# Performance work log

Measured on AMD Instinct MI355X. Metric: run time of the kernel, lower is better.

The kernel has to match this reference:

```python
import jax, jax.numpy as jnp
import numpy as np

D = 1024
HEADS = 16
HEAD_DIM = D // HEADS
B = 4
L = 1024


def setup_inputs() -> dict:
    key = jax.random.key(0)
    kq, kk, kv, kw, kb = jax.random.split(key, 5)
    Q = jax.random.normal(kq, (B, L, D), dtype=jnp.float32)
    K = jax.random.normal(kk, (B, L, D), dtype=jnp.float32)
    V = jax.random.normal(kv, (B, L, D), dtype=jnp.float32)
    # Output projection H: torch nn.Linear(D, D) -> weight (D, D), bias (D,)
    lim = 1.0 / np.sqrt(D)
    W_H = jax.random.uniform(kw, (D, D), minval=-lim, maxval=lim, dtype=jnp.float32)
    b_H = jax.random.uniform(kb, (D,), minval=-lim, maxval=lim, dtype=jnp.float32)
    mask = 0  # falsy -> no masking branch, matching `if mask` in the source
    return {"Q": Q, "K": K, "V": V, "W_H": W_H, "b_H": b_H, "mask": mask}


def reference(Q, K, V, W_H, b_H, mask):
    batch, q_len, _ = Q.shape
    k_len = K.shape[1]
    Qh = Q.reshape(batch, q_len, HEADS, HEAD_DIM)
    Kh = K.reshape(batch, k_len, HEADS, HEAD_DIM)
    Vh = V.reshape(batch, k_len, HEADS, HEAD_DIM)
    scores = jnp.einsum('bqhd,bkhd->bhqk', Qh, Kh)  # [B,H,Lq,Lk]
    if mask:  # mask is a Python scalar (0 -> skip), as in source
        scores = jnp.where(mask == 0, -jnp.inf, scores)
    # NOTE: source scales by sqrt(D), not sqrt(head_dim)
    attn = jax.nn.softmax(scores / np.sqrt(D).astype(np.float32), axis=3)
    out = jnp.einsum('bhql,blhd->bqhd', attn, Vh).reshape(batch, q_len, D)
    return out @ W_H.T + b_H
```

## Files before the change

kernel.cpp:

```cpp
#include <hip/hip_runtime.h>
#include <hip/hip_bf16.h>

typedef __attribute__((ext_vector_type(4))) float f32x4;
typedef __attribute__((ext_vector_type(8))) short bf16x8;

constexpr int Bn  = 4;
constexpr int Ln  = 1024;
constexpr int Dn  = 1024;
constexpr int Hn  = 16;
constexpr int HDn = 64;

static __device__ __forceinline__ unsigned short bf16r(float f) {
    union { float f; unsigned int u; } x;
    x.f = f;
    unsigned int r = x.u + 0x7fffu + ((x.u >> 16) & 1u);
    return (unsigned short)(r >> 16);
}

static __device__ __forceinline__ unsigned int pk2(float a, float b) {
    return (unsigned int)bf16r(a) | ((unsigned int)bf16r(b) << 16);
}

__global__ __launch_bounds__(256) void prep_kernel(
    const float* __restrict__ Vg, const float* __restrict__ Wg,
    unsigned short* __restrict__ Vtg, unsigned short* __restrict__ Wbf)
{
    const int tid = threadIdx.x;
    if (blockIdx.z == 4) {
        const int r0 = blockIdx.x * 64, c0 = blockIdx.y * 64;
#pragma unroll 4
        for (int i = 0; i < 4; ++i) {
            int e4 = i * 256 + tid;
            int r = e4 >> 4, c4 = e4 & 15;
            const float* p = Wg + (size_t)(r0 + r) * Dn + c0 + c4 * 4;
            float4 v = *(const float4*)p;
            ushort4 o;
            o.x = bf16r(v.x); o.y = bf16r(v.y); o.z = bf16r(v.z); o.w = bf16r(v.w);
            *(ushort4*)(Wbf + (size_t)(r0 + r) * Dn + c0 + c4 * 4) = o;
        }
        return;
    }

    __shared__ unsigned short T[64][72];
    const int k0 = blockIdx.x * 64;
    const int h  = blockIdx.y;
    const int b  = blockIdx.z;
    const float* Vb = Vg + (size_t)b * Ln * Dn + h * HDn;

#pragma unroll 4
    for (int i = 0; i < 4; ++i) {
        int e4 = i * 256 + tid;
        int r = e4 >> 4, c4 = e4 & 15;
        float4 vv = *(const float4*)(Vb + (size_t)(k0 + r) * Dn + c4 * 4);
        T[c4 * 4 + 0][r] = bf16r(vv.x);
        T[c4 * 4 + 1][r] = bf16r(vv.y);
        T[c4 * 4 + 2][r] = bf16r(vv.z);
        T[c4 * 4 + 3][r] = bf16r(vv.w);
    }
    __syncthreads();
    unsigned short* out = Vtg + ((size_t)(b * Hn + h) * HDn) * Ln + k0;
#pragma unroll 2
    for (int i = 0; i < 2; ++i) {
        int e8 = i * 256 + tid;
        int r = e8 >> 3, c8 = e8 & 7;
        *(uint4*)(out + (size_t)r * Ln + c8 * 8) = *(const uint4*)&T[r][c8 * 8];
    }
}

__global__ __launch_bounds__(512) void attn_kernel(
    const float* __restrict__ Qg, const float* __restrict__ Kg,
    const unsigned short* __restrict__ Vtg, unsigned short* __restrict__ Xg)
{
    __shared__ uint4 Ks4[2][64][8];
    __shared__ uint4 Vts4[2][64][8];
    __shared__ uint2 Ps2[256][16];

    const int tid  = threadIdx.x;
    const int wave = tid >> 6;
    const int lane = tid & 63;
    const int l16  = lane & 15;
    const int quad = lane >> 4;
    const int r7   = l16 & 7;
    const int wb   = wave * 32;

    const int flat = blockIdx.x;
    const int xcd  = flat & 7;
    const int j    = flat >> 3;
    const int qt   = j & 3;
    const int gg   = j >> 2;
    const int g    = xcd + 8 * gg;
    const int h    = g & 15;
    const int b    = g >> 4;
    const int q0   = qt * 256;

    const float* Kf   = Kg + (size_t)b * Ln * Dn + h * HDn;
    const uint4* Vtb4 = (const uint4*)(Vtg + ((size_t)(b * Hn + h) * HDn) * Ln);

    bf16x8 bq[2][2];
#pragma unroll 2
    for (int hf = 0; hf < 2; ++hf) {
        const float* qp = Qg + ((size_t)b * Ln + q0 + wb + hf * 16 + l16) * Dn
                             + h * HDn + quad * 8;
        float4 a0 = *(const float4*)qp;
        float4 a1 = *(const float4*)(qp + 4);
        float4 a2 = *(const float4*)(qp + 32);
        float4 a3 = *(const float4*)(qp + 36);
        bq[hf][0][0] = (short)bf16r(a0.x); bq[hf][0][1] = (short)bf16r(a0.y);
        bq[hf][0][2] = (short)bf16r(a0.z); bq[hf][0][3] = (short)bf16r(a0.w);
        bq[hf][0][4] = (short)bf16r(a1.x); bq[hf][0][5] = (short)bf16r(a1.y);
        bq[hf][0][6] = (short)bf16r(a1.z); bq[hf][0][7] = (short)bf16r(a1.w);
        bq[hf][1][0] = (short)bf16r(a2.x); bq[hf][1][1] = (short)bf16r(a2.y);
        bq[hf][1][2] = (short)bf16r(a2.z); bq[hf][1][3] = (short)bf16r(a2.w);
        bq[hf][1][4] = (short)bf16r(a3.x); bq[hf][1][5] = (short)bf16r(a3.y);
        bq[hf][1][6] = (short)bf16r(a3.z); bq[hf][1][7] = (short)bf16r(a3.w);
    }

    const float SC = 1.4426950408889634f / 32.0f;

    float lsum[2] = {0.f, 0.f};
    f32x4 Oacc[2][4];
#pragma unroll 2
    for (int hf = 0; hf < 2; ++hf)
#pragma unroll 4
        for (int d = 0; d < 4; ++d) Oacc[hf][d] = (f32x4){0.f, 0.f, 0.f, 0.f};

    const int sr = tid >> 3, sc = tid & 7;
    const int scs = sc ^ (sr & 7);
    float4 kr0, kr1;
    uint4 vreg;

    kr0 = *(const float4*)(Kf + (size_t)sr * Dn + sc * 8);
    kr1 = *(const float4*)(Kf + (size_t)sr * Dn + sc * 8 + 4);
    vreg = Vtb4[(size_t)sr * 128 + sc];
    Ks4[0][sr][scs] = (uint4){pk2(kr0.x, kr0.y), pk2(kr0.z, kr0.w),
                              pk2(kr1.x, kr1.y), pk2(kr1.z, kr1.w)};
    Vts4[0][sr][scs] = vreg;
    kr0 = *(const float4*)(Kf + (size_t)(64 + sr) * Dn + sc * 8);
    kr1 = *(const float4*)(Kf + (size_t)(64 + sr) * Dn + sc * 8 + 4);
    vreg = Vtb4[(size_t)sr * 128 + 8 + sc];
    __syncthreads();

    constexpr int NT = Ln / 64;
    for (int it = 0; it < NT; ++it) {
        const int cur = it & 1;

        f32x4 st[2][4];
        __builtin_amdgcn_s_setprio(1);
#pragma unroll 4
        for (int n = 0; n < 4; ++n) {
            bf16x8 a0 = __builtin_bit_cast(bf16x8, Ks4[cur][n * 16 + l16][quad ^ r7]);
            bf16x8 a1 = __builtin_bit_cast(bf16x8, Ks4[cur][n * 16 + l16][(4 + quad) ^ r7]);
#pragma unroll 2
            for (int hf = 0; hf < 2; ++hf) {
                f32x4 acc = (f32x4){0.f, 0.f, 0.f, 0.f};
                acc = __builtin_amdgcn_mfma_f32_16x16x32_bf16(a0, bq[hf][0], acc, 0, 0, 0);
                acc = __builtin_amdgcn_mfma_f32_16x16x32_bf16(a1, bq[hf][1], acc, 0, 0, 0);
                st[hf][n] = acc;
            }
        }
        __builtin_amdgcn_s_setprio(0);

#pragma unroll 2
        for (int hf = 0; hf < 2; ++hf) {
            float ls = 0.f;
#pragma unroll 4
            for (int n = 0; n < 4; ++n) {
                float p0 = __builtin_amdgcn_exp2f(st[hf][n][0] * SC);
                float p1 = __builtin_amdgcn_exp2f(st[hf][n][1] * SC);
                float p2 = __builtin_amdgcn_exp2f(st[hf][n][2] * SC);
                float p3 = __builtin_amdgcn_exp2f(st[hf][n][3] * SC);
                ls += (p0 + p1) + (p2 + p3);
                uint2 w;
                w.x = pk2(p0, p1);
                w.y = pk2(p2, p3);
                Ps2[wb + hf * 16 + l16][(n * 4 + quad) ^ (r7 << 1)] = w;
            }
            lsum[hf] += ls;
        }

        __builtin_amdgcn_s_setprio(1);
#pragma unroll 2
        for (int kk = 0; kk < 2; ++kk) {
            bf16x8 bv[4];
#pragma unroll 4
            for (int dt = 0; dt < 4; ++dt)
                bv[dt] = __builtin_bit_cast(bf16x8,
                    Vts4[cur][dt * 16 + l16][(kk * 4 + quad) ^ r7]);
#pragma unroll 2
            for (int hf = 0; hf < 2; ++hf) {
                int blk = (kk * 4 + quad) ^ r7;
                bf16x8 ap = *(const bf16x8*)&Ps2[wb + hf * 16 + l16][blk * 2];
#pragma unroll 4
                for (int dt = 0; dt < 4; ++dt)
                    Oacc[hf][dt] = __builtin_amdgcn_mfma_f32_16x16x32_bf16(
                        ap, bv[dt], Oacc[hf][dt], 0, 0, 0);
            }
        }
        __builtin_amdgcn_s_setprio(0);

        if (it + 1 < NT) {
            Ks4[cur ^ 1][sr][scs] = (uint4){pk2(kr0.x, kr0.y), pk2(kr0.z, kr0.w),
                                            pk2(kr1.x, kr1.y), pk2(kr1.z, kr1.w)};
            Vts4[cur ^ 1][sr][scs] = vreg;
            if (it + 2 < NT) {
                kr0 = *(const float4*)(Kf + (size_t)((it + 2) * 64 + sr) * Dn + sc * 8);
                kr1 = *(const float4*)(Kf + (size_t)((it + 2) * 64 + sr) * Dn + sc * 8 + 4);
                vreg = Vtb4[(size_t)sr * 128 + (it + 2) * 8 + sc];
            }
        }
        __syncthreads();
    }

    float inv[2];
#pragma unroll 2
    for (int hf = 0; hf < 2; ++hf) {
        float rs = lsum[hf];
        rs += __shfl_xor(rs, 16, 64);
        rs += __shfl_xor(rs, 32, 64);
        inv[hf] = __builtin_amdgcn_rcpf(rs);
    }

    unsigned short* Xb = Xg + ((size_t)b * Ln + q0 + wb) * Dn + h * HDn;
#pragma unroll 2
    for (int hf = 0; hf < 2; ++hf)
#pragma unroll 4
        for (int r = 0; r < 4; ++r) {
            float iv = __shfl(inv[hf], quad * 4 + r, 64);
            int row = hf * 16 + quad * 4 + r;
#pragma unroll 4
            for (int dt = 0; dt < 4; ++dt)
                Xb[(size_t)row * Dn + dt * 16 + l16] = bf16r(Oacc[hf][dt][r] * iv);
        }
}

__global__ __launch_bounds__(256) void proj_kernel(
    const unsigned short* __restrict__ Xg, const unsigned short* __restrict__ Wbf,
    const float* __restrict__ bg, float* __restrict__ Yg)
{
    __shared__ unsigned short XsL[128 * 64];
    __shared__ unsigned short WsL[64 * 64];

    const int tid  = threadIdx.x;
    const int wave = tid >> 6;
    const int lane = tid & 63;
    const int l16  = lane & 15;
    const int quad = lane >> 4;
    const int mw   = (wave & 1) * 64;
    const int nw   = (wave >> 1) * 32;

    const int m0 = blockIdx.x * 128;
    const int n0 = blockIdx.y * 64;

    f32x4 acc[4][2];
#pragma unroll 4
    for (int mt = 0; mt < 4; ++mt)
#pragma unroll 2
        for (int nt = 0; nt < 2; ++nt)
            acc[mt][nt] = (f32x4){0.f, 0.f, 0.f, 0.f};

    for (int it = 0; it < Dn / 64; ++it) {
        const int kk0 = it * 64;
        __syncthreads();
#pragma unroll 4
        for (int i = 0; i < 4; ++i) {
            int fl = i * 256 + tid;
            int r = fl >> 3, c8 = fl & 7;
            __builtin_amdgcn_global_load_lds(
                (const __attribute__((address_space(1))) void*)
                    (Xg + (size_t)(m0 + r) * Dn + kk0 + c8 * 8),
                (__attribute__((address_space(3))) void*)&XsL[fl * 8],
                16, 0, 0);
        }
#pragma unroll 2
        for (int i = 0; i < 2; ++i) {
            int fl = i * 256 + tid;
            int r = fl >> 3, c8 = fl & 7;
            __builtin_amdgcn_global_load_lds(
                (const __attribute__((address_space(1))) void*)
                    (Wbf + (size_t)(n0 + r) * Dn + kk0 + c8 * 8),
                (__attribute__((address_space(3))) void*)&WsL[fl * 8],
                16, 0, 0);
        }
        __syncthreads();

        __builtin_amdgcn_s_setprio(1);
#pragma unroll 2
        for (int ks = 0; ks < 2; ++ks) {
            bf16x8 af[4], bfr[2];
#pragma unroll 4
            for (int mt = 0; mt < 4; ++mt)
                af[mt] = *(const bf16x8*)&XsL[(mw + mt * 16 + l16) * 64 + ks * 32 + quad * 8];
#pragma unroll 2
            for (int nt = 0; nt < 2; ++nt)
                bfr[nt] = *(const bf16x8*)&WsL[(nw + nt * 16 + l16) * 64 + ks * 32 + quad * 8];
#pragma unroll 4
            for (int mt = 0; mt < 4; ++mt)
#pragma unroll 2
                for (int nt = 0; nt < 2; ++nt)
                    acc[mt][nt] = __builtin_amdgcn_mfma_f32_16x16x32_bf16(
                        af[mt], bfr[nt], acc[mt][nt], 0, 0, 0);
        }
        __builtin_amdgcn_s_setprio(0);
    }

#pragma unroll 2
    for (int nt = 0; nt < 2; ++nt) {
        int col = n0 + nw + nt * 16 + l16;
        float bb = bg[col];
#pragma unroll 4
        for (int mt = 0; mt < 4; ++mt)
#pragma unroll 4
            for (int r = 0; r < 4; ++r) {
                int row = m0 + mw + mt * 16 + quad * 4 + r;
                Yg[(size_t)row * Dn + col] = acc[mt][nt][r] + bb;
            }
    }
}

extern "C" void kernel_launch(void* const* d_in, const int* in_sizes, int n_in,
                              void* d_out, int out_size, void* d_ws, size_t ws_size,
                              hipStream_t stream) {
    const float* Q    = (const float*)d_in[0];
    const float* K    = (const float*)d_in[1];
    const float* V    = (const float*)d_in[2];
    const float* W    = (const float*)d_in[3];
    const float* bias = (const float*)d_in[4];

    unsigned short* Vt  = (unsigned short*)d_ws;
    unsigned short* Wbf = Vt + (size_t)Bn * Ln * Dn;
    unsigned short* X   = Wbf + (size_t)Dn * Dn;
    float* Y = (float*)d_out;

    dim3 gp(Ln / 64, Hn, Bn + 1);
    prep_kernel<<<gp, 256, 0, stream>>>(V, W, Vt, Wbf);

    attn_kernel<<<dim3(256, 1, 1), 512, 0, stream>>>(Q, K, Vt, X);

    dim3 g2(Bn * Ln / 128, Dn / 64);
    proj_kernel<<<g2, 256, 0, stream>>>(X, Wbf, bias, Y);
}
```

Before: 144.8 us.

## Double-buffer projection GEMM LDS tiles and shrink M tile to 64

The output projection kernel now uses two LDS buffers so the global-to-LDS loads for the next K slice are issued before the MFMA work on the current slice, overlapping memory with compute. The M tile drops from 128 to 64 rows, which doubles the grid to 1024 blocks for better occupancy across CUs but lowers per-block data reuse. There is one barrier per iteration instead of two. Correctness depends on global_load_lds completing before the end-of-iteration barrier, which is not explicitly waited on.

After: 144.4 us. About the same (-0.3%).

```diff
diff --git a/kernel.cpp b/kernel.cpp
--- a/kernel.cpp
+++ b/kernel.cpp
@@ -237,78 +237,95 @@
     const unsigned short* __restrict__ Xg, const unsigned short* __restrict__ Wbf,
     const float* __restrict__ bg, float* __restrict__ Yg)
 {
-    __shared__ unsigned short XsL[128 * 64];
-    __shared__ unsigned short WsL[64 * 64];
+    __shared__ unsigned short XsL[2][64 * 64];
+    __shared__ unsigned short WsL[2][64 * 64];
 
     const int tid  = threadIdx.x;
     const int wave = tid >> 6;
     const int lane = tid & 63;
     const int l16  = lane & 15;
     const int quad = lane >> 4;
-    const int mw   = (wave & 1) * 64;
+    const int mw   = (wave & 1) * 32;
     const int nw   = (wave >> 1) * 32;
 
-    const int m0 = blockIdx.x * 128;
+    const int m0 = blockIdx.x * 64;
     const int n0 = blockIdx.y * 64;
 
-    f32x4 acc[4][2];
-#pragma unroll 4
-    for (int mt = 0; mt < 4; ++mt)
+    f32x4 acc[2][2];
+#pragma unroll 2
+    for (int mt = 0; mt < 2; ++mt)
 #pragma unroll 2
         for (int nt = 0; nt < 2; ++nt)
             acc[mt][nt] = (f32x4){0.f, 0.f, 0.f, 0.f};
 
-    for (int it = 0; it < Dn / 64; ++it) {
-        const int kk0 = it * 64;
-        __syncthreads();
-#pragma unroll 4
-        for (int i = 0; i < 4; ++i) {
-            int fl = i * 256 + tid;
-            int r = fl >> 3, c8 = fl & 7;
-            __builtin_amdgcn_global_load_lds(
-                (const __attribute__((address_space(1))) void*)
-                    (Xg + (size_t)(m0 + r) * Dn + kk0 + c8 * 8),
-                (__attribute__((address_space(3))) void*)&XsL[fl * 8],
-                16, 0, 0);
-        }
-#pragma unroll 2
-        for (int i = 0; i < 2; ++i) {
-            int fl = i * 256 + tid;
-            int r = fl >> 3, c8 = fl & 7;
-            __builtin_amdgcn_global_load_lds(
-                (const __attribute__((address_space(1))) void*)
-                    (Wbf + (size_t)(n0 + r) * Dn + kk0 + c8 * 8),
-                (__attribute__((address_space(3))) void*)&WsL[fl * 8],
-                16, 0, 0);
-        }
-        __syncthreads();
+#pragma unroll 2
+    for (int i = 0; i < 2; ++i) {
+        int fl = i * 256 + tid;
+        int r = fl >> 3, c8 = fl & 7;
+        __builtin_amdgcn_global_load_lds(
+            (const __attribute__((address_space(1))) void*)
+                (Xg + (size_t)(m0 + r) * Dn + c8 * 8),
+            (__attribute__((address_space(3))) void*)&XsL[0][fl * 8], 16, 0, 0);
+        __builtin_amdgcn_global_load_lds(
+            (const __attribute__((address_space(1))) void*)
+                (Wbf + (size_t)(n0 + r) * Dn + c8 * 8),
+            (__attribute__((address_space(3))) void*)&WsL[0][fl * 8], 16, 0, 0);
+    }
+    __syncthreads();
+
+    constexpr int NI = Dn / 64;
+    for (int it = 0; it < NI; ++it) {
+        const int cur = it & 1;
+
+        if (it + 1 < NI) {
+            const int kk1 = (it + 1) * 64;
+#pragma unroll 2
+            for (int i = 0; i < 2; ++i) {
+                int fl = i * 256 + tid;
+                int r = fl >> 3, c8 = fl & 7;
+                __builtin_amdgcn_global_load_lds(
+                    (const __attribute__((address_space(1))) void*)
+                        (Xg + (size_t)(m0 + r) * Dn + kk1 + c8 * 8),
+                    (__attribute__((address_space(3))) void*)&XsL[cur ^ 1][fl * 8],
+                    16, 0, 0);
+                __builtin_amdgcn_global_load_lds(
+                    (const __attribute__((address_space(1))) void*)
+                        (Wbf + (size_t)(n0 + r) * Dn + kk1 + c8 * 8),
+                    (__attribute__((address_space(3))) void*)&WsL[cur ^ 1][fl * 8],
+                    16, 0, 0);
+            }
+        }
 
         __builtin_amdgcn_s_setprio(1);
 #pragma unroll 2
         for (int ks = 0; ks < 2; ++ks) {
-            bf16x8 af[4], bfr[2];
-#pragma unroll 4
-            for (int mt = 0; mt < 4; ++mt)
-                af[mt] = *(const bf16x8*)&XsL[(mw + mt * 16 + l16) * 64 + ks * 32 + quad * 8];
+            bf16x8 af[2], bfr[2];
+#pragma unroll 2
+            for (int mt = 0; mt < 2; ++mt)
+                af[mt] = *(const bf16x8*)&XsL[cur][(mw + mt * 16 + l16) * 64
+                                                  + ks * 32 + quad * 8];
 #pragma unroll 2
             for (int nt = 0; nt < 2; ++nt)
-                bfr[nt] = *(const bf16x8*)&WsL[(nw + nt * 16 + l16) * 64 + ks * 32 + quad * 8];
-#pragma unroll 4
-            for (int mt = 0; mt < 4; ++mt)
+                bfr[nt] = *(const bf16x8*)&WsL[cur][(nw + nt * 16 + l16) * 64
+                                                   + ks * 32 + quad * 8];
+#pragma unroll 2
+            for (int mt = 0; mt < 2; ++mt)
 #pragma unroll 2
                 for (int nt = 0; nt < 2; ++nt)
                     acc[mt][nt] = __builtin_amdgcn_mfma_f32_16x16x32_bf16(
                         af[mt], bfr[nt], acc[mt][nt], 0, 0, 0);
         }
         __builtin_amdgcn_s_setprio(0);
+
+        __syncthreads();
     }
 
 #pragma unroll 2
     for (int nt = 0; nt < 2; ++nt) {
         int col = n0 + nw + nt * 16 + l16;
         float bb = bg[col];
-#pragma unroll 4
-        for (int mt = 0; mt < 4; ++mt)
+#pragma unroll 2
+        for (int mt = 0; mt < 2; ++mt)
 #pragma unroll 4
             for (int r = 0; r < 4; ++r) {
                 int row = m0 + mw + mt * 16 + quad * 4 + r;
@@ -336,6 +353,6 @@
 
     attn_kernel<<<dim3(256, 1, 1), 512, 0, stream>>>(Q, K, Vt, X);
 
-    dim3 g2(Bn * Ln / 128, Dn / 64);
+    dim3 g2(Bn * Ln / 64, Dn / 64);
     proj_kernel<<<g2, 256, 0, stream>>>(X, Wbf, bias, Y);
 }
```
